# Kernel tuning notes

Measured on AMD Instinct MI355X. Metric: run time of the kernel, lower is better.

Reference implementation:

```python
import jax, jax.numpy as jnp
import numpy as np

LAMBDA_S = 1.0   # options['lambda_s']
NITER = 100      # options['iter_ihs']

_HS_FILTER = jnp.array([[1/12, 1/6, 1/12],
                        [1/6,  0.0, 1/6 ],
                        [1/12, 1/6, 1/12]], dtype=jnp.float32)


def _smooth(f):
    # f: [n, h, w] -> 3x3 Horn-Schunck weighted average, zero padding (== torch conv2d padding=1)
    k = _HS_FILTER.reshape(1, 1, 3, 3)  # [out_c, in_c, kh, kw]
    return jax.lax.conv_general_dilated(f[:, None], k, window_strides=(1, 1), padding='SAME')[:, 0]


def setup_inputs() -> dict:
    key = jax.random.key(0)
    k1, k2 = jax.random.split(key)
    n, h, w = 8, 256, 256
    x = jax.random.normal(k1, (n, 3, h, w), dtype=jnp.float32)            # [I_t, I_x, I_y]
    old_estimate = jax.random.normal(k2, (n, 2, h, w), dtype=jnp.float32)  # warm-start (u, v)
    return {"x": x, "old_estimate": old_estimate}


def reference(x, old_estimate):
    # x: [n,3,h,w]; old_estimate: [n,2,h,w]
    I_t, I_x, I_y = x[:, 0], x[:, 1], x[:, 2]
    denom = LAMBDA_S ** 2 + I_x ** 2 + I_y ** 2  # iteration-invariant
    u0, v0 = old_estimate[:, 0], old_estimate[:, 1]  # warm_ihs=True

    def step(carry, _):
        u, v = carry
        u_bar = _smooth(u)
        v_bar = _smooth(v)
        der = (I_x * u_bar + I_y * v_bar + I_t) / denom
        return (u_bar - I_x * der, v_bar - I_y * der), None

    (u, v), _ = jax.lax.scan(step, (u0, v0), None, length=NITER)
    return jnp.stack((u, v), axis=1)  # [n,2,h,w]
```

## Files before the change

kernel.cpp:

```cpp
#include <hip/hip_runtime.h>

typedef unsigned long long ull;
typedef float f32x2 __attribute__((ext_vector_type(2)));
#define FMA2(a,b,c) __builtin_elementwise_fma((a),(b),(c))

#define HH 256
#define WW 256
#define PLANE (HH*WW)
#define TILE_R 32
#define TILE_C 64
#define TT 8
#define ER (TILE_R + 2*TT)
#define EC (TILE_C + 2*TT)
#define NCP (EC/2)
#define NRG 16
#define RPT (ER/NRG)
#define NTHR 1024
#define STRIDE 164
#define LSZ (4 + ER*STRIDE + 4)

#define RING_OFS (2u*1024u*1024u)
#define FLAG_OFS (4u*1024u*1024u)
#define RIMG (HH*(WW/2)*4)
#define NBLK 256

__device__ __forceinline__ float dpp_prev(float v) {
    return __int_as_float(__builtin_amdgcn_update_dpp(0, __float_as_int(v), 0x138, 0xF, 0xF, true));
}
__device__ __forceinline__ float dpp_next(float v) {
    return __int_as_float(__builtin_amdgcn_update_dpp(0, __float_as_int(v), 0x130, 0xF, 0xF, true));
}

__device__ __forceinline__ void hsum2(const float4 M, f32x2& S0, f32x2& S1) {
    f32x2 lo = { M.x, M.y }, hi = { M.z, M.w };
    f32x2 DL = { dpp_prev(M.z), dpp_prev(M.w) };
    f32x2 DR = { dpp_next(M.x), dpp_next(M.y) };
    const f32x2 two = 2.0f;
    S0 = FMA2(two, lo, DL) + hi;
    S1 = FMA2(two, hi, lo) + DR;
}

__device__ __forceinline__ void hs_step(
    const float* __restrict__ rbuf, float* __restrict__ wbuf,
    int fb, int rm, int rw0, int rN, bool fullwb,
    float4* __restrict__ Mreg,
    const f32x2 (* __restrict__ CA)[2], const f32x2 (* __restrict__ CB)[2],
    const f32x2 (* __restrict__ CC)[2])
{
    float4 Mb0 = *(const float4*)(rbuf + STRIDE*rm + fb);
    float4 MbN = *(const float4*)(rbuf + STRIDE*rN + fb);

    f32x2 S0[RPT+2], S1[RPT+2];
    #pragma unroll
    for (int j = 0; j < RPT; ++j) hsum2(Mreg[j], S0[j+1], S1[j+1]);
    hsum2(Mb0, S0[0], S1[0]);
    hsum2(MbN, S0[RPT+1], S1[RPT+1]);

    const f32x2 two = 2.0f, m4 = -4.0f;
    #pragma unroll
    for (int j = 0; j < RPT; ++j) {
        float4 Mc = Mreg[j];
        f32x2 Mlo = { Mc.x, Mc.y }, Mhi = { Mc.z, Mc.w };
        f32x2 T0 = FMA2(m4, Mlo, FMA2(two, S0[j+1], S0[j]) + S0[j+2]);
        f32x2 T1 = FMA2(m4, Mhi, FMA2(two, S1[j+1], S1[j]) + S1[j+2]);
        f32x2 rr0 = FMA2(CA[j][0], T0, -FMA2(CB[j][0], T0.yx, CC[j][0]));
        f32x2 rr1 = FMA2(CA[j][1], T1, -FMA2(CB[j][1], T1.yx, CC[j][1]));
        float4 nv = make_float4(rr0.x, rr0.y, rr1.x, rr1.y);
        Mreg[j] = nv;
        if (j == 0 || j == RPT-1 || fullwb)
            *(float4*)(wbuf + STRIDE*(rw0 + j) + fb) = nv;
    }
}

__global__ __launch_bounds__(NTHR, 4)
void hs_mega(const float* __restrict__ x,
             const float* __restrict__ est,
             float* __restrict__ out,
             float* __restrict__ ws)
{
    __shared__ __align__(16) float s0[LSZ];
    __shared__ __align__(16) float s1[LSZ];

    const int img = blockIdx.x, cs = blockIdx.y, rb = blockIdx.z;
    const int tid = threadIdx.x;
    const int er0 = rb*TILE_R - TT;
    const int ec0 = cs*TILE_C - TT;
    const int blin = (img*4 + cs)*8 + rb;
    unsigned* flags = (unsigned*)(ws + FLAG_OFS);

    int nb = -1;
    if (tid < 8) {
        int t = (tid < 4) ? tid : tid + 1;
        int dr = t/3 - 1, dc = t%3 - 1;
        int nrb = rb + dr, ncs = cs + dc;
        if (nrb >= 0 && nrb < 8 && ncs >= 0 && ncs < 4)
            nb = (img*4 + ncs)*8 + nrb;
    }

    const int cp = tid & 63;
    const int rg = tid >> 6;
    const bool act = (cp < NCP);
    const int r0 = rg * RPT;
    const int fb = 4 + 4*cp;
    const int rm = (r0 == 0) ? 0 : r0 - 1;
    const int rN = (r0 + RPT > ER-1) ? ER-1 : r0+RPT;

    f32x2 CA[RPT][2], CB[RPT][2], CC[RPT][2];
    if (act) {
        const float* __restrict__ xit = x + img*3*PLANE;
        const float* __restrict__ xix = xit + PLANE;
        const float* __restrict__ xiy = xix + PLANE;
        #pragma unroll
        for (int i = 0; i < RPT; ++i) {
            int gr = er0 + r0 + i;
            #pragma unroll
            for (int j = 0; j < 2; ++j) {
                int gc = ec0 + 2*cp + j;
                float A=0.f, B=0.f, C=0.f, D=0.f, E=0.f;
                if (gr >= 0 && gr < HH && gc >= 0 && gc < WW) {
                    int q = gr*WW + gc;
                    float it = xit[q], ix = xix[q], iy = xiy[q];
                    float rd = 1.0f / (1.0f + ix*ix + iy*iy);
                    const float s12 = 1.0f/12.0f;
                    A = (1.0f - ix*ix*rd) * s12;
                    B = (ix*iy*rd) * s12;
                    C = ix*it*rd;
                    D = (1.0f - iy*iy*rd) * s12;
                    E = iy*it*rd;
                }
                CA[i][j] = (f32x2){ A, D };
                CB[i][j] = (f32x2){ B, B };
                CC[i][j] = (f32x2){ C, E };
            }
        }
    }

    {
        const float* __restrict__ eu = est + img*2*PLANE;
        const float* __restrict__ ev = eu + PLANE;
        for (int k = tid; k < ER*NCP; k += NTHR) {
            int r = k / NCP, c = k - r*NCP;
            int gr = er0 + r, gc = ec0 + 2*c;
            float2 uu = make_float2(0.f,0.f), vv = make_float2(0.f,0.f);
            if (gr >= 0 && gr < HH && gc >= 0 && gc < WW) {
                uu = *(const float2*)(eu + gr*WW + gc);
                vv = *(const float2*)(ev + gr*WW + gc);
            }
            *(float4*)(s0 + 4 + STRIDE*r + 4*c) = make_float4(uu.x, vv.x, uu.y, vv.y);
        }
    }
    __syncthreads();

    float4 Mreg[RPT];
    if (act) {
        #pragma unroll
        for (int j = 0; j < RPT; ++j)
            Mreg[j] = *(const float4*)(s0 + STRIDE*(r0 + j) + fb);
    }

    for (int p = 0; p < 13; ++p) {
        if (p < 12) {
            #pragma unroll
            for (int q = 0; q < 4; ++q) {
                if (act) hs_step(s0, s1, fb, rm, r0, rN, false, Mreg, CA, CB, CC);
                __syncthreads();
                if (act) hs_step(s1, s0, fb, rm, r0, rN, (q == 3), Mreg, CA, CB, CC);
                __syncthreads();
            }
        } else {
            #pragma unroll
            for (int q = 0; q < 2; ++q) {
                if (act) hs_step(s0, s1, fb, rm, r0, rN, false, Mreg, CA, CB, CC);
                __syncthreads();
                if (act) hs_step(s1, s0, fb, rm, r0, rN, (q == 1), Mreg, CA, CB, CC);
                __syncthreads();
            }
        }

        if (p < 12) {
            float* ring = ws + (unsigned)(p & 1) * RING_OFS + img*RIMG;

            for (int k = tid; k < 640; k += NTHR) {
                int m = k; int r, c2;
                if (m < 256)      { r = m >> 5;              c2 = m & 31; }
                else if (m < 512) { r = 24 + ((m-256) >> 5); c2 = (m-256) & 31; }
                else { int mm = m - 512; r = 8 + (mm >> 3); int t = mm & 7; c2 = (t < 4) ? t : 24 + t; }
                const float* sp = s0 + 4 + STRIDE*(r + TT) + 4*(c2 + 4);
                float* gp = ring + ((rb*TILE_R + r)*(WW/2) + cs*(TILE_C/2) + c2)*4;
                __hip_atomic_store((ull*)gp,     *(const ull*)sp,       __ATOMIC_RELAXED, __HIP_MEMORY_SCOPE_AGENT);
                __hip_atomic_store((ull*)gp + 1, *(const ull*)(sp + 2), __ATOMIC_RELAXED, __HIP_MEMORY_SCOPE_AGENT);
            }
            asm volatile("s_waitcnt vmcnt(0)" ::: "memory");
            __syncthreads();
            if (tid == 0)
                __hip_atomic_store(&flags[p*NBLK + blin], 0x5eed0100u + (unsigned)p,
                                   __ATOMIC_RELAXED, __HIP_MEMORY_SCOPE_AGENT);
            asm volatile("" ::: "memory");
            if (tid < 8 && nb >= 0) {
                const unsigned tgt = 0x5eed0100u + (unsigned)p;
                while (__hip_atomic_load(&flags[p*NBLK + nb],
                                         __ATOMIC_RELAXED, __HIP_MEMORY_SCOPE_AGENT) != tgt)
                    __builtin_amdgcn_s_sleep(1);
            }
            __syncthreads();

            for (int k = tid; k < 896; k += NTHR) {
                int m = k; int r, c2;
                if (m < 320)      { r = m / 40;              c2 = m - (m/40)*40; }
                else if (m < 640) { int mm = m-320; r = 40 + mm/40; c2 = mm - (mm/40)*40; }
                else { int mm = m - 640; r = 8 + (mm >> 3); int t = mm & 7; c2 = (t < 4) ? t : 32 + t; }
                int gr = er0 + r, gc2 = cs*(TILE_C/2) - 4 + c2;
                ull v0 = 0, v1 = 0;
                if (gr >= 0 && gr < HH && gc2 >= 0 && gc2 < WW/2) {
                    const float* gp = ring + (gr*(WW/2) + gc2)*4;
                    v0 = __hip_atomic_load((const ull*)gp,     __ATOMIC_RELAXED, __HIP_MEMORY_SCOPE_AGENT);
                    v1 = __hip_atomic_load((const ull*)gp + 1, __ATOMIC_RELAXED, __HIP_MEMORY_SCOPE_AGENT);
                }
                float* sp = s0 + 4 + STRIDE*r + 4*c2;
                *(ull*)sp = v0;
                *(ull*)(sp + 2) = v1;
            }
            __syncthreads();

            if (act) {
                #pragma unroll
                for (int j = 0; j < RPT; ++j) {
                    int r = r0 + j;
                    if (r < TT || r >= ER-TT || cp < 4 || cp >= NCP-4)
                        Mreg[j] = *(const float4*)(s0 + STRIDE*r + fb);
                }
            }
        }
    }

    {
        float* ou = out + img*2*PLANE;
        float* ov = ou + PLANE;
        for (int k = tid; k < 1024; k += NTHR) {
            int r = k >> 5, c2 = k & 31;
            float4 V = *(const float4*)(s0 + 4 + STRIDE*(r + TT) + 4*(c2 + 4));
            int q = (rb*TILE_R + r)*WW + cs*TILE_C + 2*c2;
            *(float2*)(ou + q) = make_float2(V.x, V.z);
            *(float2*)(ov + q) = make_float2(V.y, V.w);
        }
    }
}

extern "C" void kernel_launch(void* const* d_in, const int* in_sizes, int n_in,
                              void* d_out, int out_size, void* d_ws, size_t ws_size,
                              hipStream_t stream) {
    const float* x   = (const float*)d_in[0];
    const float* est = (const float*)d_in[1];
    float* out = (float*)d_out;
    float* ws  = (float*)d_ws;

    dim3 grid(8, WW/TILE_C, HH/TILE_R);
    dim3 blk(NTHR);
    hs_mega<<<grid, blk, 0, stream>>>(x, est, out, ws);
}
```

Measured before the change: 167.5 us.

## Exchange horizontal partial sums between row groups and skip dead halo rows

Instead of double-buffering the whole tile in LDS and reading neighbour rows to recompute horizontal sums, each row group now publishes the horizontal sums of its first and last rows into a small LDS exchange buffer. Neighbouring groups read those, which removes the second full tile buffer and the redundant boundary hsum work. Row groups whose rows fall outside the shrinking valid region at step q are switched off. One barrier per step is kept, and an extra barrier is added after each sweep. Edge handling changes at the outer edge of the extended tile (rows are replicated rather than clamped), which is acceptable only because those halo rows are discarded.

```diff
diff --git a/kernel.cpp b/kernel.cpp
--- a/kernel.cpp
+++ b/kernel.cpp
@@ -18,6 +18,8 @@
 #define NTHR 1024
 #define STRIDE 164
 #define LSZ (4 + ER*STRIDE + 4)
+#define HROW (NCP*4)
+#define HBUFSZ (2*NRG*2*HROW)
 
 #define RING_OFS (2u*1024u*1024u)
 #define FLAG_OFS (4u*1024u*1024u)
@@ -40,35 +42,49 @@
     S1 = FMA2(two, hi, lo) + DR;
 }
 
-__device__ __forceinline__ void hs_step(
-    const float* __restrict__ rbuf, float* __restrict__ wbuf,
-    int fb, int rm, int rw0, int rN, bool fullwb,
+__device__ __forceinline__ void do_step(
+    int q, int S, float* __restrict__ sraw, float* __restrict__ hbuf,
+    bool act, int rg, int cp, int r0, int fb,
     float4* __restrict__ Mreg,
     const f32x2 (* __restrict__ CA)[2], const f32x2 (* __restrict__ CB)[2],
     const f32x2 (* __restrict__ CC)[2])
 {
-    float4 Mb0 = *(const float4*)(rbuf + STRIDE*rm + fb);
-    float4 MbN = *(const float4*)(rbuf + STRIDE*rN + fb);
-
+    const int par = (q - 1) & 1;
+    const bool on = act && (r0 + RPT - 1 >= q - 1) && (r0 <= 48 - q);
     f32x2 S0[RPT+2], S1[RPT+2];
-    #pragma unroll
-    for (int j = 0; j < RPT; ++j) hsum2(Mreg[j], S0[j+1], S1[j+1]);
-    hsum2(Mb0, S0[0], S1[0]);
-    hsum2(MbN, S0[RPT+1], S1[RPT+1]);
-
-    const f32x2 two = 2.0f, m4 = -4.0f;
-    #pragma unroll
-    for (int j = 0; j < RPT; ++j) {
-        float4 Mc = Mreg[j];
-        f32x2 Mlo = { Mc.x, Mc.y }, Mhi = { Mc.z, Mc.w };
-        f32x2 T0 = FMA2(m4, Mlo, FMA2(two, S0[j+1], S0[j]) + S0[j+2]);
-        f32x2 T1 = FMA2(m4, Mhi, FMA2(two, S1[j+1], S1[j]) + S1[j+2]);
-        f32x2 rr0 = FMA2(CA[j][0], T0, -FMA2(CB[j][0], T0.yx, CC[j][0]));
-        f32x2 rr1 = FMA2(CA[j][1], T1, -FMA2(CB[j][1], T1.yx, CC[j][1]));
-        float4 nv = make_float4(rr0.x, rr0.y, rr1.x, rr1.y);
-        Mreg[j] = nv;
-        if (j == 0 || j == RPT-1 || fullwb)
-            *(float4*)(wbuf + STRIDE*(rw0 + j) + fb) = nv;
+
+    if (on) {
+        #pragma unroll
+        for (int j = 0; j < RPT; ++j) hsum2(Mreg[j], S0[j+1], S1[j+1]);
+        float* hb = hbuf + (par*NRG + rg)*2*HROW + 4*cp;
+        *(float4*)(hb)        = make_float4(S0[1].x,   S0[1].y,   S1[1].x,   S1[1].y);
+        *(float4*)(hb + HROW) = make_float4(S0[RPT].x, S0[RPT].y, S1[RPT].x, S1[RPT].y);
+    }
+    __syncthreads();
+    if (on) {
+        if (rg > 0) {
+            float4 t = *(const float4*)(hbuf + ((par*NRG + rg-1)*2 + 1)*HROW + 4*cp);
+            S0[0] = (f32x2){t.x, t.y}; S1[0] = (f32x2){t.z, t.w};
+        } else { S0[0] = S0[1]; S1[0] = S1[1]; }
+        if (rg < NRG-1) {
+            float4 t = *(const float4*)(hbuf + ((par*NRG + rg+1)*2 + 0)*HROW + 4*cp);
+            S0[RPT+1] = (f32x2){t.x, t.y}; S1[RPT+1] = (f32x2){t.z, t.w};
+        } else { S0[RPT+1] = S0[RPT]; S1[RPT+1] = S1[RPT]; }
+
+        const f32x2 two = 2.0f, m4 = -4.0f;
+        const bool fullwb = (q == S);
+        #pragma unroll
+        for (int j = 0; j < RPT; ++j) {
+            float4 Mc = Mreg[j];
+            f32x2 Mlo = { Mc.x, Mc.y }, Mhi = { Mc.z, Mc.w };
+            f32x2 T0 = FMA2(m4, Mlo, FMA2(two, S0[j+1], S0[j]) + S0[j+2]);
+            f32x2 T1 = FMA2(m4, Mhi, FMA2(two, S1[j+1], S1[j]) + S1[j+2]);
+            f32x2 rr0 = FMA2(CA[j][0], T0, -FMA2(CB[j][0], T0.yx, CC[j][0]));
+            f32x2 rr1 = FMA2(CA[j][1], T1, -FMA2(CB[j][1], T1.yx, CC[j][1]));
+            float4 nv = make_float4(rr0.x, rr0.y, rr1.x, rr1.y);
+            Mreg[j] = nv;
+            if (fullwb) *(float4*)(sraw + STRIDE*(r0 + j) + fb) = nv;
+        }
     }
 }
 
@@ -78,8 +94,8 @@
              float* __restrict__ out,
              float* __restrict__ ws)
 {
-    __shared__ __align__(16) float s0[LSZ];
-    __shared__ __align__(16) float s1[LSZ];
+    __shared__ __align__(16) float sraw[LSZ];
+    __shared__ __align__(16) float hbuf[HBUFSZ];
 
     const int img = blockIdx.x, cs = blockIdx.y, rb = blockIdx.z;
     const int tid = threadIdx.x;
@@ -102,8 +118,6 @@
     const bool act = (cp < NCP);
     const int r0 = rg * RPT;
     const int fb = 4 + 4*cp;
-    const int rm = (r0 == 0) ? 0 : r0 - 1;
-    const int rN = (r0 + RPT > ER-1) ? ER-1 : r0+RPT;
 
     f32x2 CA[RPT][2], CB[RPT][2], CC[RPT][2];
     if (act) {
@@ -146,7 +160,7 @@
                 uu = *(const float2*)(eu + gr*WW + gc);
                 vv = *(const float2*)(ev + gr*WW + gc);
             }
-            *(float4*)(s0 + 4 + STRIDE*r + 4*c) = make_float4(uu.x, vv.x, uu.y, vv.y);
+            *(float4*)(sraw + 4 + STRIDE*r + 4*c) = make_float4(uu.x, vv.x, uu.y, vv.y);
         }
     }
     __syncthreads();
@@ -155,27 +169,20 @@
     if (act) {
         #pragma unroll
         for (int j = 0; j < RPT; ++j)
-            Mreg[j] = *(const float4*)(s0 + STRIDE*(r0 + j) + fb);
+            Mreg[j] = *(const float4*)(sraw + STRIDE*(r0 + j) + fb);
     }
 
     for (int p = 0; p < 13; ++p) {
         if (p < 12) {
             #pragma unroll
-            for (int q = 0; q < 4; ++q) {
-                if (act) hs_step(s0, s1, fb, rm, r0, rN, false, Mreg, CA, CB, CC);
-                __syncthreads();
-                if (act) hs_step(s1, s0, fb, rm, r0, rN, (q == 3), Mreg, CA, CB, CC);
-                __syncthreads();
-            }
+            for (int q = 1; q <= 8; ++q)
+                do_step(q, 8, sraw, hbuf, act, rg, cp, r0, fb, Mreg, CA, CB, CC);
         } else {
             #pragma unroll
-            for (int q = 0; q < 2; ++q) {
-                if (act) hs_step(s0, s1, fb, rm, r0, rN, false, Mreg, CA, CB, CC);
-                __syncthreads();
-                if (act) hs_step(s1, s0, fb, rm, r0, rN, (q == 1), Mreg, CA, CB, CC);
-                __syncthreads();
-            }
-        }
+            for (int q = 1; q <= 4; ++q)
+                do_step(q, 4, sraw, hbuf, act, rg, cp, r0, fb, Mreg, CA, CB, CC);
+        }
+        __syncthreads();
 
         if (p < 12) {
             float* ring = ws + (unsigned)(p & 1) * RING_OFS + img*RIMG;
@@ -185,7 +192,7 @@
                 if (m < 256)      { r = m >> 5;              c2 = m & 31; }
                 else if (m < 512) { r = 24 + ((m-256) >> 5); c2 = (m-256) & 31; }
                 else { int mm = m - 512; r = 8 + (mm >> 3); int t = mm & 7; c2 = (t < 4) ? t : 24 + t; }
-                const float* sp = s0 + 4 + STRIDE*(r + TT) + 4*(c2 + 4);
+                const float* sp = sraw + 4 + STRIDE*(r + TT) + 4*(c2 + 4);
                 float* gp = ring + ((rb*TILE_R + r)*(WW/2) + cs*(TILE_C/2) + c2)*4;
                 __hip_atomic_store((ull*)gp,     *(const ull*)sp,       __ATOMIC_RELAXED, __HIP_MEMORY_SCOPE_AGENT);
                 __hip_atomic_store((ull*)gp + 1, *(const ull*)(sp + 2), __ATOMIC_RELAXED, __HIP_MEMORY_SCOPE_AGENT);
@@ -216,7 +223,7 @@
                     v0 = __hip_atomic_load((const ull*)gp,     __ATOMIC_RELAXED, __HIP_MEMORY_SCOPE_AGENT);
                     v1 = __hip_atomic_load((const ull*)gp + 1, __ATOMIC_RELAXED, __HIP_MEMORY_SCOPE_AGENT);
                 }
-                float* sp = s0 + 4 + STRIDE*r + 4*c2;
+                float* sp = sraw + 4 + STRIDE*r + 4*c2;
                 *(ull*)sp = v0;
                 *(ull*)(sp + 2) = v1;
             }
@@ -227,7 +234,7 @@
                 for (int j = 0; j < RPT; ++j) {
                     int r = r0 + j;
                     if (r < TT || r >= ER-TT || cp < 4 || cp >= NCP-4)
-                        Mreg[j] = *(const float4*)(s0 + STRIDE*r + fb);
+                        Mreg[j] = *(const float4*)(sraw + STRIDE*r + fb);
                 }
             }
         }
@@ -238,7 +245,7 @@
         float* ov = ou + PLANE;
         for (int k = tid; k < 1024; k += NTHR) {
             int r = k >> 5, c2 = k & 31;
-            float4 V = *(const float4*)(s0 + 4 + STRIDE*(r + TT) + 4*(c2 + 4));
+            float4 V = *(const float4*)(sraw + 4 + STRIDE*(r + TT) + 4*(c2 + 4));
             int q = (rb*TILE_R + r)*WW + cs*TILE_C + 2*c2;
             *(float2*)(ou + q) = make_float2(V.x, V.z);
             *(float2*)(ov + q) = make_float2(V.y, V.w);
```

Measured after the change: 170.1 us. No clear change (+1.6%).
